# Performance work log

Measured on AMD Instinct MI355X. Metric: run time of the kernel, lower is better.

Reference implementation:

```python
import math
import jax, jax.numpy as jnp
import numpy as np

B, S, E, H = 4, 2048, 2048, 16
D = E // H
EPSILON, DELTA, MAX_GRAD_NORM = 1.0, 1e-05, 1.0
# Gaussian mechanism calibration: sigma = C * sqrt(2 ln(1.25/delta)) / epsilon
NOISE_SCALE = MAX_GRAD_NORM * math.sqrt(2.0 * math.log(1.25 / DELTA)) / EPSILON


def _xavier(key, fan_in, fan_out):
    lim = math.sqrt(6.0 / (fan_in + fan_out))
    return jax.random.uniform(key, (fan_out, fan_in), jnp.float32, -lim, lim)


def setup_inputs() -> dict:
    key = jax.random.key(0)
    ks = jax.random.split(key, 8)
    return {
        'query': jax.random.normal(ks[0], (B, S, E), jnp.float32),
        'key_t': jax.random.normal(ks[1], (B, S, E), jnp.float32),
        'value': jax.random.normal(ks[2], (B, S, E), jnp.float32),
        'Wq': _xavier(ks[3], E, E), 'bq': jnp.zeros((E,), jnp.float32),
        'Wk': _xavier(ks[4], E, E), 'bk': jnp.zeros((E,), jnp.float32),
        'Wv': _xavier(ks[5], E, E), 'bv': jnp.zeros((E,), jnp.float32),
        'Wo': _xavier(ks[6], E, E), 'bo': jnp.zeros((E,), jnp.float32),
        'noise': jax.random.normal(ks[7], (B, S, E), jnp.float32),
    }


def reference(query, key_t, value, Wq, bq, Wk, bk, Wv, bv, Wo, bo, noise):
    b, s, e = query.shape
    scale = 1.0 / math.sqrt(D)
    # QKV projections (torch Linear: x @ W.T + b) -> [b, s, H, D]
    q = (query @ Wq.T + bq).reshape(b, s, H, D)
    k = (key_t @ Wk.T + bk).reshape(b, s, H, D)
    v = (value @ Wv.T + bv).reshape(b, s, H, D)
    # attention scores [b, H, s, s]
    scores = jnp.einsum('bqhd,bkhd->bhqk', q, k) * scale
    attn = jax.nn.softmax(scores, axis=-1)
    ctx = jnp.einsum('bhqk,bkhd->bqhd', attn, v).reshape(b, s, e)
    # DP noise injected inside the kernel on the attention output
    ctx = ctx + noise * NOISE_SCALE
    # output projection
    return ctx @ Wo.T + bo
```

## Files before the change

### kernel.cpp

```cpp
#include <hip/hip_runtime.h>
#include <cmath>

#define BATCH 4
#define SEQ   2048
#define EMB   2048
#define NH    16
#define HD    128
#define MDIM  (BATCH*SEQ)
#define KDIM  EMB
#define NDIM  EMB

typedef __bf16 bf16x8 __attribute__((ext_vector_type(8)));
typedef float  f32x4  __attribute__((ext_vector_type(4)));

__device__ __forceinline__ ushort bf16rne(float f) {
  unsigned u = __builtin_bit_cast(unsigned, f);
  u += 0x7fffu + ((u >> 16) & 1u);
  return (ushort)(u >> 16);
}

__global__ __launch_bounds__(256) void cvt_bf16(const float* __restrict__ in,
                                                ushort* __restrict__ out) {
  int i = (blockIdx.x * 256 + threadIdx.x) * 4;
  float4 v = *(const float4*)(in + i);
  ushort4 o;
  o.x = bf16rne(v.x); o.y = bf16rne(v.y); o.z = bf16rne(v.z); o.w = bf16rne(v.w);
  *(ushort4*)(out + i) = o;
}

template<int MODE>
__global__ __launch_bounds__(256, 2)
void gemm_nt(const ushort* __restrict__ A, const ushort* __restrict__ Bm,
             const float* __restrict__ bias, void* __restrict__ out) {
  __shared__ ushort As[128][72];
  __shared__ ushort Bs[128][72];

  const int tid  = threadIdx.x;
  const int wave = tid >> 6, lane = tid & 63;
  const int l15  = lane & 15, quad = lane >> 4;
  const int m0 = blockIdx.x * 128, n0 = blockIdx.y * 128;
  const int wr = (wave >> 1) * 64, wc = (wave & 1) * 64;

  const f32x4 zero4 = {0.f, 0.f, 0.f, 0.f};
  f32x4 acc[4][4];
#pragma unroll
  for (int i = 0; i < 4; ++i)
#pragma unroll
    for (int j = 0; j < 4; ++j) acc[i][j] = zero4;

  for (int kk = 0; kk < KDIM; kk += 64) {
#pragma unroll
    for (int it = 0; it < 4; ++it) {
      int L = it * 256 + tid;
      int row = L >> 3, c8 = (L & 7) * 8;
      int4 va = *(const int4*)(A  + (size_t)(m0 + row) * KDIM + kk + c8);
      int4 vb = *(const int4*)(Bm + (size_t)(n0 + row) * KDIM + kk + c8);
      *(int4*)(&As[row][c8]) = va;
      *(int4*)(&Bs[row][c8]) = vb;
    }
    __syncthreads();
#pragma unroll
    for (int ks = 0; ks < 2; ++ks) {
      bf16x8 af[4], bfr[4];
#pragma unroll
      for (int i = 0; i < 4; ++i)
        af[i] = __builtin_bit_cast(bf16x8, *(const int4*)(&As[wr + i*16 + l15][ks*32 + quad*8]));
#pragma unroll
      for (int j = 0; j < 4; ++j)
        bfr[j] = __builtin_bit_cast(bf16x8, *(const int4*)(&Bs[wc + j*16 + l15][ks*32 + quad*8]));
#pragma unroll
      for (int i = 0; i < 4; ++i)
#pragma unroll
        for (int j = 0; j < 4; ++j)
          acc[i][j] = __builtin_amdgcn_mfma_f32_16x16x32_bf16(af[i], bfr[j], acc[i][j], 0, 0, 0);
    }
    __syncthreads();
  }

  if constexpr (MODE == 0) {
    float* O = (float*)out;
#pragma unroll
    for (int i = 0; i < 4; ++i)
#pragma unroll
      for (int j = 0; j < 4; ++j) {
        int n = n0 + wc + j*16 + l15;
        float bb = bias[n];
#pragma unroll
        for (int r = 0; r < 4; ++r) {
          int m = m0 + wr + i*16 + quad*4 + r;
          O[(size_t)m * NDIM + n] = acc[i][j][r] + bb;
        }
      }
  } else if constexpr (MODE == 1) {
    ushort* O = (ushort*)out;
#pragma unroll
    for (int i = 0; i < 4; ++i)
#pragma unroll
      for (int j = 0; j < 4; ++j) {
        int n = n0 + wc + j*16 + l15;
        float bb = bias[n];
        int h = n >> 7, d = n & 127;
#pragma unroll
        for (int r = 0; r < 4; ++r) {
          int m = m0 + wr + i*16 + quad*4 + r;
          int b = m >> 11, srow = m & 2047;
          O[(((size_t)(b*NH + h) * SEQ + srow) << 7) + d] = bf16rne(acc[i][j][r] + bb);
        }
      }
  } else {
    __shared__ float Tt[4][16][17];
    ushort* O = (ushort*)out;
    const int h = n0 >> 7;
#pragma unroll
    for (int i = 0; i < 4; ++i)
#pragma unroll
      for (int j = 0; j < 4; ++j) {
        int n = n0 + wc + j*16 + l15;
        float bb = bias[n];
#pragma unroll
        for (int r = 0; r < 4; ++r)
          Tt[wave][l15][quad*4 + r] = acc[i][j][r] + bb;
#pragma unroll
        for (int r = 0; r < 4; ++r) {
          int dl = quad*4 + r, sl = l15;
          float v = Tt[wave][dl][sl];
          int m = m0 + wr + i*16 + sl;
          int b = m >> 11, srow = m & 2047;
          int d = wc + j*16 + dl;
          O[((size_t)(b*NH + h) * HD + d) * SEQ + srow] = bf16rne(v);
        }
      }
  }
}

__global__ __launch_bounds__(256, 2)
void attn_kernel(const ushort* __restrict__ Qh, const ushort* __restrict__ Kh,
                 const ushort* __restrict__ Vt, const float* __restrict__ noise,
                 ushort* __restrict__ ctxn, float scale, float ns) {
  __shared__ ushort Ks[64][136];
  __shared__ ushort Vs[128][72];
  __shared__ ushort Ps[64][72];

  const int tid  = threadIdx.x;
  const int wave = tid >> 6, lane = tid & 63;
  const int l15  = lane & 15, quad = lane >> 4;
  const int q0 = blockIdx.x * 64;
  const int bh = blockIdx.y;
  const int b  = bh >> 4, h = bh & 15;

  bf16x8 qf[4];
  {
    const int qrow = q0 + wave*16 + l15;
    const ushort* qp = Qh + ((size_t)bh * SEQ + qrow) * HD;
#pragma unroll
    for (int ks = 0; ks < 4; ++ks)
      qf[ks] = __builtin_bit_cast(bf16x8, *(const int4*)(qp + ks*32 + quad*8));
  }

  const f32x4 zero4 = {0.f, 0.f, 0.f, 0.f};
  f32x4 o[8];
#pragma unroll
  for (int nb = 0; nb < 8; ++nb) o[nb] = zero4;
  float rs[4] = {0.f, 0.f, 0.f, 0.f};

  for (int k0 = 0; k0 < SEQ; k0 += 64) {
#pragma unroll
    for (int it = 0; it < 4; ++it) {
      int L = it * 256 + tid;
      int r = L >> 4, c8 = (L & 15) * 8;
      *(int4*)(&Ks[r][c8]) = *(const int4*)(Kh + ((size_t)bh * SEQ + k0 + r) * HD + c8);
    }
#pragma unroll
    for (int it = 0; it < 4; ++it) {
      int L = it * 256 + tid;
      int r = L >> 3, c8 = (L & 7) * 8;
      *(int4*)(&Vs[r][c8]) = *(const int4*)(Vt + ((size_t)bh * HD + r) * SEQ + k0 + c8);
    }
    __syncthreads();

#pragma unroll
    for (int ct = 0; ct < 4; ++ct) {
      f32x4 s = zero4;
#pragma unroll
      for (int ks = 0; ks < 4; ++ks) {
        bf16x8 kf = __builtin_bit_cast(bf16x8, *(const int4*)(&Ks[ct*16 + l15][ks*32 + quad*8]));
        s = __builtin_amdgcn_mfma_f32_16x16x32_bf16(qf[ks], kf, s, 0, 0, 0);
      }
#pragma unroll
      for (int r = 0; r < 4; ++r) {
        float p = __expf(s[r] * scale);
        rs[r] += p;
        Ps[wave*16 + quad*4 + r][ct*16 + l15] = bf16rne(p);
      }
    }

#pragma unroll
    for (int ks2 = 0; ks2 < 2; ++ks2) {
      bf16x8 pa = __builtin_bit_cast(bf16x8, *(const int4*)(&Ps[wave*16 + l15][ks2*32 + quad*8]));
#pragma unroll
      for (int nb = 0; nb < 8; ++nb) {
        bf16x8 vb = __builtin_bit_cast(bf16x8, *(const int4*)(&Vs[nb*16 + l15][ks2*32 + quad*8]));
        o[nb] = __builtin_amdgcn_mfma_f32_16x16x32_bf16(pa, vb, o[nb], 0, 0, 0);
      }
    }
    __syncthreads();
  }

#pragma unroll
  for (int r = 0; r < 4; ++r) {
    float v = rs[r];
    v += __shfl_xor(v, 1);
    v += __shfl_xor(v, 2);
    v += __shfl_xor(v, 4);
    v += __shfl_xor(v, 8);
    rs[r] = v;
  }

#pragma unroll
  for (int r = 0; r < 4; ++r) {
    float inv = 1.0f / rs[r];
    int sg = q0 + wave*16 + quad*4 + r;
    size_t rowbase = ((size_t)(b * SEQ + sg)) * EMB + h * HD;
#pragma unroll
    for (int nb = 0; nb < 8; ++nb) {
      int e = nb*16 + l15;
      float val = o[nb][r] * inv + noise[rowbase + e] * ns;
      ctxn[rowbase + e] = bf16rne(val);
    }
  }
}

extern "C" void kernel_launch(void* const* d_in, const int* in_sizes, int n_in,
                              void* d_out, int out_size, void* d_ws, size_t ws_size,
                              hipStream_t stream) {
  const float* query = (const float*)d_in[0];
  const float* key_t = (const float*)d_in[1];
  const float* value = (const float*)d_in[2];
  const float* Wq = (const float*)d_in[3];
  const float* bq = (const float*)d_in[4];
  const float* Wk = (const float*)d_in[5];
  const float* bk = (const float*)d_in[6];
  const float* Wv = (const float*)d_in[7];
  const float* bv = (const float*)d_in[8];
  const float* Wo = (const float*)d_in[9];
  const float* bo = (const float*)d_in[10];
  const float* noise = (const float*)d_in[11];

  const size_t SZ_ACT = (size_t)MDIM * KDIM * 2;
  const size_t SZ_W   = (size_t)NDIM * KDIM * 2;
  const size_t need_full = 7 * SZ_ACT + 4 * SZ_W;

  char* p = (char*)d_ws;
  ushort *qb, *kb;
  if (ws_size >= need_full) {
    qb = (ushort*)p; p += SZ_ACT;
    kb = (ushort*)p; p += SZ_ACT;
  } else {
    qb = (ushort*)d_out;
    kb = (ushort*)((char*)d_out + SZ_ACT);
  }
  ushort* vb   = (ushort*)p; p += SZ_ACT;
  ushort* wqb  = (ushort*)p; p += SZ_W;
  ushort* wkb  = (ushort*)p; p += SZ_W;
  ushort* wvb  = (ushort*)p; p += SZ_W;
  ushort* wob  = (ushort*)p; p += SZ_W;
  ushort* Qh   = (ushort*)p; p += SZ_ACT;
  ushort* Kh   = (ushort*)p; p += SZ_ACT;
  ushort* Vt   = (ushort*)p; p += SZ_ACT;
  ushort* ctxn = (ushort*)p; p += SZ_ACT;

  const int nAct = MDIM * KDIM;
  const int nW   = NDIM * KDIM;
  const float NS = (float)sqrt(2.0 * log(1.25 / 1e-5));
  const float SCALE = (float)(1.0 / sqrt((double)HD));

  cvt_bf16<<<dim3(nAct / 1024), dim3(256), 0, stream>>>(query, qb);
  cvt_bf16<<<dim3(nAct / 1024), dim3(256), 0, stream>>>(key_t, kb);
  cvt_bf16<<<dim3(nAct / 1024), dim3(256), 0, stream>>>(value, vb);
  cvt_bf16<<<dim3(nW / 1024),   dim3(256), 0, stream>>>(Wq, wqb);
  cvt_bf16<<<dim3(nW / 1024),   dim3(256), 0, stream>>>(Wk, wkb);
  cvt_bf16<<<dim3(nW / 1024),   dim3(256), 0, stream>>>(Wv, wvb);
  cvt_bf16<<<dim3(nW / 1024),   dim3(256), 0, stream>>>(Wo, wob);

  dim3 ggrid(MDIM / 128, NDIM / 128);
  gemm_nt<1><<<ggrid, dim3(256), 0, stream>>>(qb, wqb, bq, (void*)Qh);
  gemm_nt<1><<<ggrid, dim3(256), 0, stream>>>(kb, wkb, bk, (void*)Kh);
  gemm_nt<2><<<ggrid, dim3(256), 0, stream>>>(vb, wvb, bv, (void*)Vt);

  attn_kernel<<<dim3(SEQ / 64, BATCH * NH), dim3(256), 0, stream>>>(
      Qh, Kh, Vt, noise, ctxn, SCALE, NS);

  gemm_nt<0><<<ggrid, dim3(256), 0, stream>>>(ctxn, wob, bo, d_out);
}
```

Before: 877.9 us.

## Register-prefetch next K/V tile and raise wave priority around MFMA blocks

The attention loop now loads the next 64-key K and V tiles from global memory into registers while the current tile is being computed, then stores them to shared memory at the top of the next iteration. The barrier is moved so the shared-memory store sits between two syncs. It also adds s_setprio around the MFMA sections so waves issuing matrix ops get scheduling priority. The aim is to hide global load latency behind compute, at the cost of 32 extra VGPRs per thread, which may hurt occupancy at the 2-blocks launch bound.

```diff
diff --git a/kernel.cpp b/kernel.cpp
--- a/kernel.cpp
+++ b/kernel.cpp
@@ -148,6 +148,12 @@
   const int bh = blockIdx.y;
   const int b  = bh >> 4, h = bh & 15;
 
+  const ushort* Kbase = Kh + (size_t)bh * SEQ * HD;
+  const ushort* Vbase = Vt + (size_t)bh * HD * SEQ;
+
+  const int rk_r = tid >> 4, rk_c = (tid & 15) * 8;
+  const int rv_r = tid >> 3, rv_c = (tid & 7) * 8;
+
   bf16x8 qf[4];
   {
     const int qrow = q0 + wave*16 + l15;
@@ -163,29 +169,45 @@
   for (int nb = 0; nb < 8; ++nb) o[nb] = zero4;
   float rs[4] = {0.f, 0.f, 0.f, 0.f};
 
+  int4 rk[4], rv[4];
+#pragma unroll
+  for (int it = 0; it < 4; ++it)
+    rk[it] = *(const int4*)(Kbase + (size_t)(it*16 + rk_r) * HD + rk_c);
+#pragma unroll
+  for (int it = 0; it < 4; ++it)
+    rv[it] = *(const int4*)(Vbase + (size_t)(it*32 + rv_r) * SEQ + rv_c);
+
   for (int k0 = 0; k0 < SEQ; k0 += 64) {
-#pragma unroll
-    for (int it = 0; it < 4; ++it) {
-      int L = it * 256 + tid;
-      int r = L >> 4, c8 = (L & 15) * 8;
-      *(int4*)(&Ks[r][c8]) = *(const int4*)(Kh + ((size_t)bh * SEQ + k0 + r) * HD + c8);
-    }
-#pragma unroll
-    for (int it = 0; it < 4; ++it) {
-      int L = it * 256 + tid;
-      int r = L >> 3, c8 = (L & 7) * 8;
-      *(int4*)(&Vs[r][c8]) = *(const int4*)(Vt + ((size_t)bh * HD + r) * SEQ + k0 + c8);
-    }
     __syncthreads();
+#pragma unroll
+    for (int it = 0; it < 4; ++it)
+      *(int4*)(&Ks[it*16 + rk_r][rk_c]) = rk[it];
+#pragma unroll
+    for (int it = 0; it < 4; ++it)
+      *(int4*)(&Vs[it*32 + rv_r][rv_c]) = rv[it];
+    __syncthreads();
+
+    if (k0 + 64 < SEQ) {
+      const ushort* kp = Kbase + (size_t)(k0 + 64) * HD;
+      const ushort* vp = Vbase + (k0 + 64);
+#pragma unroll
+      for (int it = 0; it < 4; ++it)
+        rk[it] = *(const int4*)(kp + (size_t)(it*16 + rk_r) * HD + rk_c);
+#pragma unroll
+      for (int it = 0; it < 4; ++it)
+        rv[it] = *(const int4*)(vp + (size_t)(it*32 + rv_r) * SEQ + rv_c);
+    }
 
 #pragma unroll
     for (int ct = 0; ct < 4; ++ct) {
       f32x4 s = zero4;
+      __builtin_amdgcn_s_setprio(1);
 #pragma unroll
       for (int ks = 0; ks < 4; ++ks) {
         bf16x8 kf = __builtin_bit_cast(bf16x8, *(const int4*)(&Ks[ct*16 + l15][ks*32 + quad*8]));
         s = __builtin_amdgcn_mfma_f32_16x16x32_bf16(qf[ks], kf, s, 0, 0, 0);
       }
+      __builtin_amdgcn_s_setprio(0);
 #pragma unroll
       for (int r = 0; r < 4; ++r) {
         float p = __expf(s[r] * scale);
@@ -194,6 +216,7 @@
       }
     }
 
+    __builtin_amdgcn_s_setprio(1);
 #pragma unroll
     for (int ks2 = 0; ks2 < 2; ++ks2) {
       bf16x8 pa = __builtin_bit_cast(bf16x8, *(const int4*)(&Ps[wave*16 + l15][ks2*32 + quad*8]));
@@ -203,7 +226,7 @@
         o[nb] = __builtin_amdgcn_mfma_f32_16x16x32_bf16(pa, vb, o[nb], 0, 0, 0);
       }
     }
-    __syncthreads();
+    __builtin_amdgcn_s_setprio(0);
   }
 
 #pragma unroll
```

After: 1.328 ms. +51.2%, slower.
